# Kernel tuning notes

Hardware: AMD Instinct MI355X
Metric: run time of the kernel (lower is better)

The kernel has to match this reference:

```python
import jax, jax.numpy as jnp
import numpy as np
import math

B, S, D_MODEL, HEADS, GRID = 4, 2048, 512, 8, 8
HEAD_DIM = D_MODEL // HEADS
A_C, K_C, C_C = 0.9724108095811765, 0.9884401790754128, 0.999449553483052


def setup_inputs() -> dict:
    key = jax.random.key(0)
    ks = jax.random.split(key, 4)
    q = jax.random.normal(ks[0], (B, S, D_MODEL), jnp.float32)
    mask = jnp.tril(jnp.ones((S, S), dtype=bool))[None, None]  # causal (1,1,S,S)
    out_dim = 3 * D_MODEL
    grid_norm = jnp.arange(1, GRID + 1, dtype=jnp.float32)  # (grid,)
    # is_first=True init: normal(0,0.4)/output_dim/grid_norm_factor
    amplitudes = jax.random.normal(ks[1], (out_dim, D_MODEL, GRID), jnp.float32) * 0.4 / out_dim / grid_norm
    # norm_freq with is_first=True -> freq = arange(1..grid) / (grid+1)**0 = arange
    freq = jnp.arange(1, GRID + 1, dtype=jnp.float32)  # (grid,)
    grid_phase = jnp.arange(1, GRID + 1, dtype=jnp.float32) / (GRID + 1)
    input_phase = jnp.linspace(0.0, math.pi, D_MODEL, dtype=jnp.float32)[:, None]  # (in,1)
    phase0 = grid_phase[None, :] + input_phase  # (in, grid)
    ratio = 1.0
    for i in range(1, GRID):
        ratio *= A_C * i ** (-K_C) + C_C
    phase = phase0 * np.float32(ratio)
    kan_bias = jnp.ones((out_dim,), jnp.float32) / out_dim
    lim = math.sqrt(6.0 / (D_MODEL + D_MODEL))  # xavier_uniform
    out_w = jax.random.uniform(ks[2], (D_MODEL, D_MODEL), jnp.float32, -lim, lim)
    out_b = jnp.zeros((D_MODEL,), jnp.float32)
    return {"q": q, "mask": mask, "freq": freq, "phase": phase,
            "amplitudes": amplitudes, "kan_bias": kan_bias,
            "out_w": out_w, "out_b": out_b}


def sinekan(x2d, freq, phase, amp, bias):
    # y[n,j] = sum_{k,l} sin(x[n,k]*f[l] + p[k,l]) * amp[j,k,l] + bias[j]
    # expand sin(a+p) = sin(a)cos(p) + cos(a)sin(p); fold phase into weights
    ang = x2d[:, :, None] * freq  # (N, in, grid)
    w_sin = amp * jnp.cos(phase)  # (out, in, grid)
    w_cos = amp * jnp.sin(phase)
    y = (jnp.einsum('nkl,jkl->nj', jnp.sin(ang), w_sin)
         + jnp.einsum('nkl,jkl->nj', jnp.cos(ang), w_cos))
    return y + bias


def rotate_half(u):
    u1, u2 = jnp.split(u, 2, axis=-1)
    return jnp.concatenate([-u2, u1], axis=-1)


def apply_rope(x, pos_emb):
    cos, sin = jnp.split(pos_emb, 2, axis=-1)  # each (S, head_dim//2)
    x_even, x_odd = x[..., ::2], x[..., 1::2]
    x1 = x_even * cos + rotate_half(x_odd) * sin
    x2 = x_odd * cos + rotate_half(x_even) * sin
    return jnp.concatenate([x1, x2], axis=-1)


def rope_emb(seq_len, dim):
    half = dim // 2
    inv_freq = 1.0 / (10000.0 ** (jnp.arange(half, dtype=jnp.float32) / half))
    ang = jnp.arange(seq_len, dtype=jnp.float32)[:, None] * inv_freq  # (S, half)
    return jnp.concatenate([jnp.cos(ang), jnp.sin(ang)], axis=-1)  # (S, dim)


def reference(q, mask, freq, phase, amplitudes, kan_bias, out_w, out_b):
    b, s, _ = q.shape
    qkv = sinekan(q.reshape(-1, D_MODEL), freq, phase, amplitudes, kan_bias)
    qkv = qkv.reshape(b, s, HEADS, 3 * HEAD_DIM).transpose(0, 2, 1, 3)  # (b,h,s,3d)
    qs, ks, vs = jnp.split(qkv, 3, axis=-1)
    pe = rope_emb(s, HEAD_DIM)
    qs = apply_rope(qs, pe)
    ks = apply_rope(ks, pe)
    scores = jnp.einsum('bhqd,bhkd->bhqk', qs, ks) / math.sqrt(HEAD_DIM)
    scores = jnp.where(mask, scores.astype(jnp.float32), -1e9)
    attn = jax.nn.softmax(scores, axis=-1)
    ctx = jnp.einsum('bhqk,bhkd->bhqd', attn, vs)
    ctx = ctx.transpose(0, 2, 1, 3).reshape(b, s, D_MODEL)
    return ctx @ out_w.T + out_b
```

## Files before the change

kernel.cpp:

```cpp
#include <hip/hip_runtime.h>
#include <math.h>


typedef __attribute__((ext_vector_type(8))) short bf16x8;
typedef __attribute__((ext_vector_type(8))) unsigned short ushort8;
typedef __attribute__((ext_vector_type(4))) unsigned short ushort4v;
typedef __attribute__((ext_vector_type(4))) float f32x4;

#define DEV __device__ __forceinline__

DEV unsigned short f2bf(float f) {
  unsigned u = __builtin_bit_cast(unsigned, f);
  u += 0x7FFFu + ((u >> 16) & 1u);
  return (unsigned short)(u >> 16);
}
DEV float bf2f(unsigned short h) {
  unsigned u = ((unsigned)h) << 16;
  return __builtin_bit_cast(float, u);
}

#define GLDS16(gp, lp)                                                         \
  __builtin_amdgcn_global_load_lds(                                            \
      (const __attribute__((address_space(1))) void*)(gp),                     \
      (__attribute__((address_space(3))) void*)(lp), 16, 0, 0)

__global__ __launch_bounds__(256) void wprep(const float* __restrict__ amp,
                                             const float* __restrict__ phase,
                                             unsigned short* __restrict__ Wb) {
  int id = blockIdx.x * 256 + threadIdx.x;
  int j = id >> 9;
  int k = id & 511;
  const float* ap = amp + (size_t)id * 8;
  const float* ph = phase + k * 8;
  union { unsigned short u[16]; uint4 v[2]; } pk;
#pragma unroll
  for (int l = 0; l < 8; ++l) {
    float sp, cp;
    sincosf(ph[l], &sp, &cp);
    float a = ap[l];
    pk.u[l] = f2bf(a * cp);
    pk.u[8 + l] = f2bf(a * sp);
  }
  uint4* dst = (uint4*)(Wb + (size_t)j * 8192 + k * 16);
  dst[0] = pk.v[0];
  dst[1] = pk.v[1];
}

__global__ __launch_bounds__(256) void owprep(const float* __restrict__ w,
                                              unsigned short* __restrict__ o) {
  int id = blockIdx.x * 256 + threadIdx.x;
  o[id] = f2bf(w[id]);
}

__global__ __launch_bounds__(256) void fgen(const float* __restrict__ q,
                                            unsigned short* __restrict__ F) {
  int id = blockIdx.x * 256 + threadIdx.x;
  int row = id >> 9;
  int dim = id & 511;
  float x = q[(size_t)row * 512 + dim];
  union { unsigned short u[16]; uint4 v[2]; } fr;
#pragma unroll
  for (int l = 1; l <= 8; ++l) {
    float a = x * (float)l;
    fr.u[l - 1] = f2bf(__sinf(a));
    fr.u[7 + l] = f2bf(__cosf(a));
  }
  uint4* dst = (uint4*)(F + (size_t)row * 8192 + dim * 16);
  dst[0] = fr.v[0];
  dst[1] = fr.v[1];
}

__global__ __launch_bounds__(512, 2) void kan_gemm8(
    const unsigned short* __restrict__ F, const unsigned short* __restrict__ Wb,
    const float* __restrict__ bias, unsigned short* __restrict__ qkv) {
  __shared__ __align__(16) char LDS[131072];

  const int tid = threadIdx.x, lane = tid & 63, wid = tid >> 6;
  const int wm = wid >> 2, wn = wid & 3;
  const int l15 = lane & 15, kg = lane >> 4;

  int bid = blockIdx.x;
  int xcd = bid & 7, u = bid >> 3;
  int mt = xcd * 4 + (u & 3), ntl = u >> 2;
  const int m0 = mt * 256, n0 = ntl * 256;

  const int rl = wid * 16 + (lane >> 3);
  const int cswz = ((lane & 7) ^ (lane >> 3)) << 4;

  f32x4 acc[8][4] = {};
  bf16x8 af[4][2], bf[2][2][2];

#define STAGE(T, PART)                                                          \
  do {                                                                          \
    const int _isB = ((PART) == 1 || (PART) == 2);                              \
    const int _half = ((PART) >= 2) ? 1 : 0;                                    \
    const int _buf = (T) & 1;                                                   \
    const char* _gb = (const char*)(_isB ? Wb : F);                             \
    size_t _grow = (size_t)((_isB ? n0 : m0) + _half * 128 + rl);               \
    char* _lb = LDS + (_isB ? 65536 : 0) + _buf * 32768 +                       \
                (_half * 128 + wid * 16) * 128;                                 \
    GLDS16(_gb + _grow * 16384 + (size_t)(T)*128 + cswz, _lb);                  \
    GLDS16(_gb + (_grow + 8) * 16384 + (size_t)(T)*128 + cswz, _lb + 1024);     \
  } while (0)

#define DSREAD_A(AB, MQ)                                                        \
  do {                                                                          \
    _Pragma("unroll") for (int mi = 0; mi < 4; ++mi)                            \
        _Pragma("unroll") for (int kk = 0; kk < 2; ++kk) {                      \
      int _r = (MQ)*128 + wm * 64 + mi * 16 + l15;                              \
      af[mi][kk] = *(const bf16x8*)((AB) + _r * 128 +                           \
                                    (((kk * 4 + kg) ^ (l15 & 7)) << 4));        \
    }                                                                           \
  } while (0)

#define DSREAD_B(BB, NQ)                                                        \
  do {                                                                          \
    _Pragma("unroll") for (int ni = 0; ni < 2; ++ni)                            \
        _Pragma("unroll") for (int kk = 0; kk < 2; ++kk) {                      \
      int _r = (NQ)*128 + wn * 32 + ni * 16 + l15;                              \
      bf[NQ][ni][kk] = *(const bf16x8*)((BB) + _r * 128 +                       \
                                        (((kk * 4 + kg) ^ (l15 & 7)) << 4));    \
    }                                                                           \
  } while (0)

#define MFMAS(MQ, NQ)                                                           \
  do {                                                                          \
    __builtin_amdgcn_s_setprio(1);                                              \
    _Pragma("unroll") for (int mi = 0; mi < 4; ++mi)                            \
        _Pragma("unroll") for (int ni = 0; ni < 2; ++ni)                        \
            _Pragma("unroll") for (int kk = 0; kk < 2; ++kk)                    \
                acc[(MQ)*4 + mi][(NQ)*2 + ni] =                                 \
        __builtin_amdgcn_mfma_f32_16x16x32_bf16(                                \
            af[mi][kk], bf[NQ][ni][kk], acc[(MQ)*4 + mi][(NQ)*2 + ni], 0, 0, 0);\
    __builtin_amdgcn_s_setprio(0);                                              \
  } while (0)

#define BAR __builtin_amdgcn_s_barrier()
#define VMW(N) asm volatile("s_waitcnt vmcnt(" #N ")" ::: "memory")
#define LGW                                                                     \
  do {                                                                          \
    asm volatile("s_waitcnt lgkmcnt(0)" ::: "memory");                          \
    __builtin_amdgcn_sched_barrier(0);                                          \
  } while (0)

  STAGE(0, 0);
  STAGE(0, 1);
  STAGE(0, 2);
  STAGE(0, 3);

#pragma unroll 2
  for (int t = 0; t < 127; ++t) {
    char* Ab = LDS + (t & 1) * 32768;
    char* Bb = LDS + 65536 + (t & 1) * 32768;
    VMW(4); BAR;
    DSREAD_A(Ab, 0); DSREAD_B(Bb, 0);
    STAGE(t + 1, 0);
    LGW; MFMAS(0, 0);
    VMW(4); BAR;
    DSREAD_B(Bb, 1);
    STAGE(t + 1, 1);
    LGW; MFMAS(0, 1);
    VMW(4); BAR;
    DSREAD_A(Ab, 1);
    STAGE(t + 1, 2);
    LGW; MFMAS(1, 0);
    BAR;
    STAGE(t + 1, 3);
    MFMAS(1, 1);
  }
  {
    char* Ab = LDS + 32768;
    char* Bb = LDS + 65536 + 32768;
    VMW(4); BAR;
    DSREAD_A(Ab, 0); DSREAD_B(Bb, 0);
    LGW; MFMAS(0, 0);
    VMW(2); BAR;
    DSREAD_B(Bb, 1);
    LGW; MFMAS(0, 1);
    VMW(0); BAR;
    DSREAD_A(Ab, 1);
    LGW; MFMAS(1, 0);
    BAR;
    MFMAS(1, 1);
  }

#pragma unroll
  for (int mq = 0; mq < 2; ++mq)
#pragma unroll
    for (int mi = 0; mi < 4; ++mi)
#pragma unroll
      for (int nq = 0; nq < 2; ++nq)
#pragma unroll
        for (int ni = 0; ni < 2; ++ni) {
          int row = m0 + mq * 128 + wm * 64 + mi * 16 + kg * 4;
          int col = n0 + nq * 128 + wn * 32 + ni * 16 + l15;
          float bv = bias[col];
          f32x4 a = acc[mq * 4 + mi][nq * 2 + ni];
#pragma unroll
          for (int j = 0; j < 4; ++j)
            qkv[(size_t)(row + j) * 1536 + col] = f2bf(a[j] + bv);
        }
#undef STAGE
#undef DSREAD_A
#undef DSREAD_B
#undef MFMAS
#undef BAR
#undef VMW
#undef LGW
}

__global__ __launch_bounds__(256) void rope_prep(const unsigned short* __restrict__ qkv,
                                                 unsigned short* __restrict__ Qr,
                                                 unsigned short* __restrict__ Kr) {
  int id = blockIdx.x * 256 + threadIdx.x;
  int i = id & 31;
  int row = id >> 5;
  int s = row & 2047;
  int bh = row >> 11;
  int b = bh >> 3, h = bh & 7;

  const unsigned short* base = qkv + ((size_t)(b * 2048 + s)) * 1536 + h * 192;

  float inv = exp2f(-(float)i * (13.287712379549449f / 32.0f));
  float ang = (float)s * inv;
  float sn, cs;
  sincosf(ang, &sn, &cs);

  int pi = (i < 16) ? i + 16 : i - 16;
  float sign = (i < 16) ? -1.f : 1.f;
  size_t orow = (size_t)row * 64;

  {
    const unsigned short* xp = base;
    float xe = bf2f(xp[2 * i]), xo = bf2f(xp[2 * i + 1]);
    float po = bf2f(xp[2 * pi + 1]), pe = bf2f(xp[2 * pi]);
    Qr[orow + i] = f2bf(xe * cs + sign * po * sn);
    Qr[orow + 32 + i] = f2bf(xo * cs + sign * pe * sn);
  }
  {
    const unsigned short* xp = base + 64;
    float xe = bf2f(xp[2 * i]), xo = bf2f(xp[2 * i + 1]);
    float po = bf2f(xp[2 * pi + 1]), pe = bf2f(xp[2 * pi]);
    Kr[orow + i] = f2bf(xe * cs + sign * po * sn);
    Kr[orow + 32 + i] = f2bf(xo * cs + sign * pe * sn);
  }
}

__global__ __launch_bounds__(256) void attn(const unsigned short* __restrict__ Qr,
                                            const unsigned short* __restrict__ Kr,
                                            const unsigned short* __restrict__ qkv,
                                            unsigned short* __restrict__ ctx) {
  __shared__ __align__(16) unsigned short Klds[32 * 64];
  __shared__ __align__(16) unsigned short Vt[64 * 36];
  __shared__ __align__(16) unsigned short Plds[4 * 512];

  const int tid = threadIdx.x;
  const int lane = tid & 63;
  const int w = tid >> 6;
  const int qb = blockIdx.x;
  const int bh = blockIdx.y;
  const int b = bh >> 3, h = bh & 7;
  const int qw = qb * 64 + w * 16;
  const int l15 = lane & 15, kg = lane >> 4;

  const unsigned short* Qp = Qr + ((size_t)bh * 2048 + qw + l15) * 64 + kg * 8;
  bf16x8 qf0 = *(const bf16x8*)Qp;
  bf16x8 qf1 = *(const bf16x8*)(Qp + 32);

  f32x4 octx[4] = {};
  float den[4] = {0.f, 0.f, 0.f, 0.f};
  unsigned short* Pw = &Plds[w * 512];

  const int skp = tid >> 3;
  const int sds = tid & 7;
  const int vd = tid & 63;
  const int vkq = tid >> 6;

  const int nkt = 2 * qb + 2;
  for (int kt = 0; kt < nkt; ++kt) {
    ushort8 kv =
        *(const ushort8*)(Kr + ((size_t)bh * 2048 + kt * 32 + skp) * 64 + sds * 8);
    *(ushort8*)((char*)Klds + ((skp * 128 + sds * 16) ^ ((skp & 7) << 4))) = kv;
    {
      const unsigned short* vcol = qkv +
          ((size_t)(b * 2048 + kt * 32 + vkq * 8)) * 1536 + h * 192 + 128 + vd;
      ushort4v lo, hi;
      lo.x = vcol[0];
      lo.y = vcol[1536];
      lo.z = vcol[2 * 1536];
      lo.w = vcol[3 * 1536];
      hi.x = vcol[4 * 1536];
      hi.y = vcol[5 * 1536];
      hi.z = vcol[6 * 1536];
      hi.w = vcol[7 * 1536];
      *(ushort4v*)&Vt[vd * 36 + vkq * 8] = lo;
      *(ushort4v*)&Vt[vd * 36 + vkq * 8 + 4] = hi;
    }
    __syncthreads();

    f32x4 zero = {0.f, 0.f, 0.f, 0.f};
#pragma unroll
    for (int f = 0; f < 2; ++f) {
      int kp = f * 16 + l15;
      int swk = (kp & 7) << 4;
      bf16x8 kf0 = *(const bf16x8*)((char*)Klds + ((kp * 128 + kg * 16) ^ swk));
      bf16x8 kf1 = *(const bf16x8*)((char*)Klds + ((kp * 128 + 64 + kg * 16) ^ swk));
      f32x4 sA = __builtin_amdgcn_mfma_f32_16x16x32_bf16(qf0, kf0, zero, 0, 0, 0);
      sA = __builtin_amdgcn_mfma_f32_16x16x32_bf16(qf1, kf1, sA, 0, 0, 0);
      int kgl = kt * 32 + kp;
#pragma unroll
      for (int j = 0; j < 4; ++j) {
        int qrow = qw + kg * 4 + j;
        float p = (kgl <= qrow) ? __expf(sA[j] * 0.125f) : 0.f;
        den[j] += p;
        int prow = kg * 4 + j;
        *(unsigned short*)((char*)Pw +
                           ((prow * 64 + kp * 2) ^ ((prow & 3) << 4))) = f2bf(p);
      }
    }
    bf16x8 pf =
        *(const bf16x8*)((char*)Pw + ((l15 * 64 + kg * 16) ^ ((l15 & 3) << 4)));
#pragma unroll
    for (int nd = 0; nd < 4; ++nd) {
      int d = nd * 16 + l15;
      union { ushort4v h[2]; bf16x8 v; } vfu;
      vfu.h[0] = *(const ushort4v*)&Vt[d * 36 + kg * 8];
      vfu.h[1] = *(const ushort4v*)&Vt[d * 36 + kg * 8 + 4];
      octx[nd] = __builtin_amdgcn_mfma_f32_16x16x32_bf16(pf, vfu.v, octx[nd], 0, 0, 0);
    }
    __syncthreads();
  }

#pragma unroll
  for (int j = 0; j < 4; ++j) {
    float d_ = den[j];
    d_ += __shfl_xor(d_, 1);
    d_ += __shfl_xor(d_, 2);
    d_ += __shfl_xor(d_, 4);
    d_ += __shfl_xor(d_, 8);
    den[j] = d_;
  }
#pragma unroll
  for (int nd = 0; nd < 4; ++nd)
#pragma unroll
    for (int j = 0; j < 4; ++j) {
      int qrow = qw + kg * 4 + j;
      int col = h * 64 + nd * 16 + l15;
      ctx[((size_t)b * 2048 + qrow) * 512 + col] = f2bf(octx[nd][j] / den[j]);
    }
}

__global__ __launch_bounds__(256) void out_gemm(const unsigned short* __restrict__ A,
                                                const unsigned short* __restrict__ Bw,
                                                const float* __restrict__ outb,
                                                float* __restrict__ out) {
  __shared__ __align__(16) unsigned short Al[128 * 32];
  __shared__ __align__(16) unsigned short Bl[128 * 32];
  const int tid = threadIdx.x, lane = tid & 63, w = tid >> 6;
  const int wm = w >> 1, wn = w & 1;
  const int m0 = blockIdx.x * 128, n0 = blockIdx.y * 128;
  const int l15 = lane & 15, kg = lane >> 4;

  f32x4 acc[4][4] = {};

  const unsigned short* ga = A + (size_t)(m0 + (tid >> 2)) * 512 + (tid & 3) * 8;
  const unsigned short* gb = Bw + (size_t)(n0 + (tid >> 2)) * 512 + (tid & 3) * 8;

  for (int t = 0; t < 16; ++t) {
    GLDS16(ga + t * 32, &Al[w * 512]);
    GLDS16(ga + t * 32 + 64 * 512, &Al[2048 + w * 512]);
    GLDS16(gb + t * 32, &Bl[w * 512]);
    GLDS16(gb + t * 32 + 64 * 512, &Bl[2048 + w * 512]);
    __syncthreads();

    bf16x8 af[4], bfr[4];
#pragma unroll
    for (int m = 0; m < 4; ++m)
      af[m] = *(const bf16x8*)&Al[(wm * 64 + m * 16 + l15) * 32 + kg * 8];
#pragma unroll
    for (int n = 0; n < 4; ++n)
      bfr[n] = *(const bf16x8*)&Bl[(wn * 64 + n * 16 + l15) * 32 + kg * 8];
#pragma unroll
    for (int m = 0; m < 4; ++m)
#pragma unroll
      for (int n = 0; n < 4; ++n)
        acc[m][n] =
            __builtin_amdgcn_mfma_f32_16x16x32_bf16(af[m], bfr[n], acc[m][n], 0, 0, 0);

    __syncthreads();
  }

  const int rb = m0 + wm * 64 + kg * 4;
  const int cb = n0 + wn * 64 + l15;
#pragma unroll
  for (int n = 0; n < 4; ++n) {
    int cc = cb + n * 16;
    float bv = outb[cc];
#pragma unroll
    for (int m = 0; m < 4; ++m)
#pragma unroll
      for (int j = 0; j < 4; ++j)
        out[(size_t)(rb + m * 16 + j) * 512 + cc] = acc[m][n][j] + bv;
  }
}

extern "C" void kernel_launch(void* const* d_in, const int* in_sizes, int n_in,
                              void* d_out, int out_size, void* d_ws, size_t ws_size,
                              hipStream_t stream) {
  const float* q = (const float*)d_in[0];
  const float* phase = (const float*)d_in[3];
  const float* amp = (const float*)d_in[4];
  const float* kbias = (const float*)d_in[5];
  const float* out_w = (const float*)d_in[6];
  const float* out_b = (const float*)d_in[7];
  float* out = (float*)d_out;

  char* p = (char*)d_ws;
  unsigned short* Wb = (unsigned short*)(p);
  unsigned short* qkv = (unsigned short*)(p + 25165824);
  unsigned short* Qr = (unsigned short*)(p + 50331648);
  unsigned short* Kr = (unsigned short*)(p + 58720256);
  unsigned short* ctx = (unsigned short*)(p + 67108864);
  unsigned short* Wob = (unsigned short*)(p + 75497472);
  unsigned short* F = (unsigned short*)(p + 76021760);

  owprep<<<1024, 256, 0, stream>>>(out_w, Wob);
  wprep<<<3072, 256, 0, stream>>>(amp, phase, Wb);
  fgen<<<16384, 256, 0, stream>>>(q, F);
  kan_gemm8<<<192, 512, 0, stream>>>(F, Wb, kbias, qkv);
  rope_prep<<<8192, 256, 0, stream>>>(qkv, Qr, Kr);
  attn<<<dim3(32, 32), 256, 0, stream>>>(Qr, Kr, qkv, ctx);
  out_gemm<<<dim3(64, 4), 256, 0, stream>>>(ctx, Wob, out_b, out);
}
```

Measured before the change: 352.9 us.

## Retile KAN GEMM to 256x192 tiles for 256 blocks

Changes the KAN projection GEMM tile from 256x256 to 256x192, which raises the block count from 192 to 256 so it matches the CU count of the chip. The staging, LDS layout, per-wave MFMA fragment shapes and the pipeline schedule are rewritten for three 16-wide N fragments per wave. The point is to fill every CU in one wave of blocks. In exchange, each tile reuses data less, so global traffic per FLOP is higher, and the revised load/wait sequencing could stall.

```diff
diff --git a/kernel.cpp b/kernel.cpp
--- a/kernel.cpp
+++ b/kernel.cpp
@@ -73,7 +73,7 @@
 __global__ __launch_bounds__(512, 2) void kan_gemm8(
     const unsigned short* __restrict__ F, const unsigned short* __restrict__ Wb,
     const float* __restrict__ bias, unsigned short* __restrict__ qkv) {
-  __shared__ __align__(16) char LDS[131072];
+  __shared__ __align__(16) char LDS[114688];
 
   const int tid = threadIdx.x, lane = tid & 63, wid = tid >> 6;
   const int wm = wid >> 2, wn = wid & 3;
@@ -81,57 +81,53 @@
 
   int bid = blockIdx.x;
   int xcd = bid & 7, u = bid >> 3;
-  int mt = xcd * 4 + (u & 3), ntl = u >> 2;
-  const int m0 = mt * 256, n0 = ntl * 256;
-
-  const int rl = wid * 16 + (lane >> 3);
+  const int m0 = (xcd * 4 + (u & 3)) * 256;
+  const int n0 = (u >> 2) * 192;
+
+  const int growl = wid * 8 + (lane >> 3);
   const int cswz = ((lane & 7) ^ (lane >> 3)) << 4;
 
-  f32x4 acc[8][4] = {};
-  bf16x8 af[4][2], bf[2][2][2];
-
-#define STAGE(T, PART)                                                          \
-  do {                                                                          \
-    const int _isB = ((PART) == 1 || (PART) == 2);                              \
-    const int _half = ((PART) >= 2) ? 1 : 0;                                    \
-    const int _buf = (T) & 1;                                                   \
-    const char* _gb = (const char*)(_isB ? Wb : F);                             \
-    size_t _grow = (size_t)((_isB ? n0 : m0) + _half * 128 + rl);               \
-    char* _lb = LDS + (_isB ? 65536 : 0) + _buf * 32768 +                       \
-                (_half * 128 + wid * 16) * 128;                                 \
-    GLDS16(_gb + _grow * 16384 + (size_t)(T)*128 + cswz, _lb);                  \
-    GLDS16(_gb + (_grow + 8) * 16384 + (size_t)(T)*128 + cswz, _lb + 1024);     \
-  } while (0)
-
-#define DSREAD_A(AB, MQ)                                                        \
+  f32x4 acc[2][4][3] = {};
+  bf16x8 af[4][2], bf[3][2];
+
+#define STAGE_A(T, C)                                                           \
+  GLDS16((const char*)F + (size_t)(m0 + (C)*64 + growl) * 16384 +               \
+             (size_t)(T) * 128 + cswz,                                          \
+         LDS + (((T)&1) * 32768 + (C)*8192 + wid * 1024))
+
+#define STAGE_B(T, C)                                                           \
+  GLDS16((const char*)Wb + (size_t)(n0 + (C)*64 + growl) * 16384 +              \
+             (size_t)(T) * 128 + cswz,                                          \
+         LDS + (65536 + ((T)&1) * 24576 + (C)*8192 + wid * 1024))
+
+#define DSREAD_A(T, MQ)                                                         \
   do {                                                                          \
     _Pragma("unroll") for (int mi = 0; mi < 4; ++mi)                            \
         _Pragma("unroll") for (int kk = 0; kk < 2; ++kk) {                      \
       int _r = (MQ)*128 + wm * 64 + mi * 16 + l15;                              \
-      af[mi][kk] = *(const bf16x8*)((AB) + _r * 128 +                           \
+      af[mi][kk] = *(const bf16x8*)(LDS + ((T)&1) * 32768 + _r * 128 +          \
                                     (((kk * 4 + kg) ^ (l15 & 7)) << 4));        \
     }                                                                           \
   } while (0)
 
-#define DSREAD_B(BB, NQ)                                                        \
+#define DSREAD_B(T)                                                             \
   do {                                                                          \
-    _Pragma("unroll") for (int ni = 0; ni < 2; ++ni)                            \
+    _Pragma("unroll") for (int ni = 0; ni < 3; ++ni)                            \
         _Pragma("unroll") for (int kk = 0; kk < 2; ++kk) {                      \
-      int _r = (NQ)*128 + wn * 32 + ni * 16 + l15;                              \
-      bf[NQ][ni][kk] = *(const bf16x8*)((BB) + _r * 128 +                       \
-                                        (((kk * 4 + kg) ^ (l15 & 7)) << 4));    \
+      int _r = wn * 48 + ni * 16 + l15;                                         \
+      bf[ni][kk] = *(const bf16x8*)(LDS + 65536 + ((T)&1) * 24576 + _r * 128 +  \
+                                    (((kk * 4 + kg) ^ (l15 & 7)) << 4));        \
     }                                                                           \
   } while (0)
 
-#define MFMAS(MQ, NQ)                                                           \
+#define MFMAS(MQ, NI0, NI1)                                                     \
   do {                                                                          \
     __builtin_amdgcn_s_setprio(1);                                              \
     _Pragma("unroll") for (int mi = 0; mi < 4; ++mi)                            \
-        _Pragma("unroll") for (int ni = 0; ni < 2; ++ni)                        \
+        _Pragma("unroll") for (int ni = (NI0); ni <= (NI1); ++ni)               \
             _Pragma("unroll") for (int kk = 0; kk < 2; ++kk)                    \
-                acc[(MQ)*4 + mi][(NQ)*2 + ni] =                                 \
-        __builtin_amdgcn_mfma_f32_16x16x32_bf16(                                \
-            af[mi][kk], bf[NQ][ni][kk], acc[(MQ)*4 + mi][(NQ)*2 + ni], 0, 0, 0);\
+                acc[MQ][mi][ni] = __builtin_amdgcn_mfma_f32_16x16x32_bf16(      \
+                    af[mi][kk], bf[ni][kk], acc[MQ][mi][ni], 0, 0, 0);          \
     __builtin_amdgcn_s_setprio(0);                                              \
   } while (0)
 
@@ -143,45 +139,39 @@
     __builtin_amdgcn_sched_barrier(0);                                          \
   } while (0)
 
-  STAGE(0, 0);
-  STAGE(0, 1);
-  STAGE(0, 2);
-  STAGE(0, 3);
+  STAGE_A(0, 0); STAGE_A(0, 1);
+  STAGE_B(0, 0); STAGE_B(0, 1); STAGE_B(0, 2);
+  STAGE_A(0, 2); STAGE_A(0, 3);
 
 #pragma unroll 2
   for (int t = 0; t < 127; ++t) {
-    char* Ab = LDS + (t & 1) * 32768;
-    char* Bb = LDS + 65536 + (t & 1) * 32768;
+    VMW(2); BAR;
+    DSREAD_A(t, 0); DSREAD_B(t);
+    STAGE_A(t + 1, 0); STAGE_A(t + 1, 1);
+    LGW; MFMAS(0, 0, 1);
+    BAR;
+    STAGE_B(t + 1, 0); STAGE_B(t + 1, 1);
+    MFMAS(0, 2, 2);
     VMW(4); BAR;
-    DSREAD_A(Ab, 0); DSREAD_B(Bb, 0);
-    STAGE(t + 1, 0);
-    LGW; MFMAS(0, 0);
-    VMW(4); BAR;
-    DSREAD_B(Bb, 1);
-    STAGE(t + 1, 1);
-    LGW; MFMAS(0, 1);
-    VMW(4); BAR;
-    DSREAD_A(Ab, 1);
-    STAGE(t + 1, 2);
-    LGW; MFMAS(1, 0);
+    DSREAD_A(t, 1);
+    STAGE_B(t + 1, 2); STAGE_A(t + 1, 2);
+    LGW; MFMAS(1, 0, 1);
     BAR;
-    STAGE(t + 1, 3);
-    MFMAS(1, 1);
+    STAGE_A(t + 1, 3);
+    MFMAS(1, 2, 2);
   }
   {
-    char* Ab = LDS + 32768;
-    char* Bb = LDS + 65536 + 32768;
-    VMW(4); BAR;
-    DSREAD_A(Ab, 0); DSREAD_B(Bb, 0);
-    LGW; MFMAS(0, 0);
+    const int t = 127;
     VMW(2); BAR;
-    DSREAD_B(Bb, 1);
-    LGW; MFMAS(0, 1);
+    DSREAD_A(t, 0); DSREAD_B(t);
+    LGW; MFMAS(0, 0, 1);
+    BAR;
+    MFMAS(0, 2, 2);
     VMW(0); BAR;
-    DSREAD_A(Ab, 1);
-    LGW; MFMAS(1, 0);
+    DSREAD_A(t, 1);
+    LGW; MFMAS(1, 0, 1);
     BAR;
-    MFMAS(1, 1);
+    MFMAS(1, 2, 2);
   }
 
 #pragma unroll
@@ -189,18 +179,17 @@
 #pragma unroll
     for (int mi = 0; mi < 4; ++mi)
 #pragma unroll
-      for (int nq = 0; nq < 2; ++nq)
-#pragma unroll
-        for (int ni = 0; ni < 2; ++ni) {
-          int row = m0 + mq * 128 + wm * 64 + mi * 16 + kg * 4;
-          int col = n0 + nq * 128 + wn * 32 + ni * 16 + l15;
-          float bv = bias[col];
-          f32x4 a = acc[mq * 4 + mi][nq * 2 + ni];
-#pragma unroll
-          for (int j = 0; j < 4; ++j)
-            qkv[(size_t)(row + j) * 1536 + col] = f2bf(a[j] + bv);
-        }
-#undef STAGE
+      for (int ni = 0; ni < 3; ++ni) {
+        int row = m0 + mq * 128 + wm * 64 + mi * 16 + kg * 4;
+        int col = n0 + wn * 48 + ni * 16 + l15;
+        float bv = bias[col];
+        f32x4 a = acc[mq][mi][ni];
+#pragma unroll
+        for (int j = 0; j < 4; ++j)
+          qkv[(size_t)(row + j) * 1536 + col] = f2bf(a[j] + bv);
+      }
+#undef STAGE_A
+#undef STAGE_B
 #undef DSREAD_A
 #undef DSREAD_B
 #undef MFMAS
@@ -427,7 +416,7 @@
   owprep<<<1024, 256, 0, stream>>>(out_w, Wob);
   wprep<<<3072, 256, 0, stream>>>(amp, phase, Wb);
   fgen<<<16384, 256, 0, stream>>>(q, F);
-  kan_gemm8<<<192, 512, 0, stream>>>(F, Wb, kbias, qkv);
+  kan_gemm8<<<256, 512, 0, stream>>>(F, Wb, kbias, qkv);
   rope_prep<<<8192, 256, 0, stream>>>(qkv, Qr, Kr);
   attn<<<dim3(32, 32), 256, 0, stream>>>(Qr, Kr, qkv, ctx);
   out_gemm<<<dim3(64, 4), 256, 0, stream>>>(ctx, Wob, out_b, out);
```

Result: faster. 319.9 us (-9.3%).
